# Performance work log

Measured on AMD Instinct MI355X. Metric: run time of the kernel, lower is better.

Reference implementation:

```python
import jax, jax.numpy as jnp
import numpy as np

EMBEDS = 195  # C, also used in the (unusual) 1/sqrt(C) scale


def setup_inputs() -> dict:
    key = jax.random.key(0)
    k1, k2, k3, k4 = jax.random.split(key, 4)
    B, T, C, H = 1024, 256, EMBEDS, 8
    x = jax.random.normal(k1, (B, T, C), dtype=jnp.float32)
    Wq = jax.random.normal(k2, (C, H), dtype=jnp.float32) * 0.05
    Wk = jax.random.normal(k3, (C, H), dtype=jnp.float32) * 0.05
    Wv = jax.random.normal(k4, (C, H), dtype=jnp.float32) * 0.05
    return {"x": x, "Wq": Wq, "Wk": Wk, "Wv": Wv}


def reference(x, Wq, Wk, Wv):
    B, T, C = x.shape
    q = jnp.einsum('btc,ch->bth', x, Wq)  # [B,T,H]
    k = jnp.einsum('btc,ch->bth', x, Wk)
    v = jnp.einsum('btc,ch->bth', x, Wv)
    # scores scaled by 1/sqrt(C) (embedding dim), faithful to source
    scores = jnp.einsum('bqh,bkh->bqk', q, k) * (1.0 / jnp.sqrt(jnp.float32(C)))
    causal = jnp.tril(jnp.ones((T, T), dtype=bool))  # [T,T]
    scores = jnp.where(causal, scores, -jnp.inf)
    attn = jax.nn.softmax(scores, axis=-1)
    # dropout treated as identity (eval mode) for deterministic reference
    out = jnp.einsum('bqk,bkh->bqh', attn, v)
    return out
```

## Files before the change

kernel.cpp:

```cpp
#include <hip/hip_runtime.h>
#include <hip/hip_bf16.h>
#include <stdint.h>

#define TT   256
#define CC   195
#define HH   8
#define NKT  7
#define VSTR 260
#define PSTR 40

typedef __attribute__((ext_vector_type(8))) short short8;
typedef __attribute__((ext_vector_type(4))) float f32x4;

static __device__ __forceinline__ short f2bf(float v) {
    union { __hip_bfloat16 h; short s; } cv;
    cv.h = __float2bfloat16(v);
    return cv.s;
}

__global__ __launch_bounds__(256, 4)
void fused_head(const float* __restrict__ x,
                const float* __restrict__ Wq,
                const float* __restrict__ Wk,
                const float* __restrict__ Wv,
                float* __restrict__ out)
{
    __shared__ short Ql[TT * 8];
    __shared__ short Kl[TT * 8];
    __shared__ short Vt[16 * VSTR];
    __shared__ short Pch[4 * 16 * PSTR];

    const int tid  = threadIdx.x;
    const int lane = tid & 63;
    const int wv   = __builtin_amdgcn_readfirstlane(tid >> 6);
    const int b    = blockIdx.x;
    const int nn   = lane & 15;
    const int quad = lane >> 4;

    {
        uint32_t* vtw = (uint32_t*)Vt;
        const int base = (8 * VSTR) / 2;
        for (int i = tid; i < (8 * VSTR) / 2; i += 256)
            vtw[base + i] = (i < VSTR / 2) ? 0x3F803F80u : 0u;
    }

    const float* __restrict__ xb = x + (size_t)b * (TT * CC);

    const float* Wsel0 = (nn < 8) ? (Wq + nn) : (Wk + nn - 8);
    const float* Wsel1 = (nn < 8) ? (Wv + nn) : nullptr;
    short8 Bf[NKT][2];
#pragma unroll
    for (int kt = 0; kt < NKT; ++kt) {
#pragma unroll
        for (int j = 0; j < 8; ++j) {
            const int k = kt * 32 + quad * 8 + j;
            float v0 = (k < CC) ? Wsel0[(size_t)k * HH] : 0.f;
            float v1 = (k < CC && Wsel1) ? Wsel1[(size_t)k * HH] : 0.f;
            Bf[kt][0][j] = f2bf(v0);
            Bf[kt][1][j] = f2bf(v1);
        }
    }

    for (int ch = 0; ch < 4; ++ch) {
        const int rbase = ch * 64 + wv * 16;
        const float* __restrict__ xrow = xb + (size_t)(rbase + nn) * CC;

        f32x4 acc0 = {0.f, 0.f, 0.f, 0.f};
        f32x4 acc1 = {0.f, 0.f, 0.f, 0.f};
#pragma unroll
        for (int kt = 0; kt < NKT; ++kt) {
            float f[8];
#pragma unroll
            for (int j = 0; j < 8; ++j) {
                const int k = kt * 32 + quad * 8 + j;
                f[j] = (k < CC) ? xrow[k] : 0.f;
            }
            short8 a;
#pragma unroll
            for (int j = 0; j < 8; ++j) a[j] = f2bf(f[j]);
            acc0 = __builtin_amdgcn_mfma_f32_16x16x32_bf16(a, Bf[kt][0], acc0, 0, 0, 0);
            acc1 = __builtin_amdgcn_mfma_f32_16x16x32_bf16(a, Bf[kt][1], acc1, 0, 0, 0);
        }
#pragma unroll
        for (int r = 0; r < 4; ++r) {
            const int trow = rbase + quad * 4 + r;
            const short qs = f2bf(acc0[r]);
            if (nn < 8) {
                Ql[trow * 8 + nn] = qs;
                Vt[nn * VSTR + trow] = f2bf(acc1[r]);
            } else {
                Kl[trow * 8 + (nn - 8)] = qs;
            }
        }
    }
    __syncthreads();

    const float SC2 = 0.07161149f * 1.44269504f;
    const int qt4[4] = { wv, 7 - wv, 8 + wv, 15 - wv };
    short* Pw = Pch + wv * (16 * PSTR);

    for (int qi = 0; qi < 4; ++qi) {
        const int qt = qt4[qi];
        const int qb = qt * 16;

        short8 aQ = (short8){0, 0, 0, 0, 0, 0, 0, 0};
        if (quad == 0)
            aQ = *reinterpret_cast<const short8*>(Ql + (qb + nn) * 8);

        f32x4 accO = {0.f, 0.f, 0.f, 0.f};
        const int nch = (qt >> 1) + 1;
        for (int c = 0; c < nch; ++c) {
            const int kb = c * 32;
            asm volatile("" ::: "memory");
#pragma unroll
            for (int half = 0; half < 2; ++half) {
                const int kb16 = kb + half * 16;
                short8 bK = (short8){0, 0, 0, 0, 0, 0, 0, 0};
                if (quad == 0)
                    bK = *reinterpret_cast<const short8*>(Kl + (kb16 + nn) * 8);
                f32x4 s = __builtin_amdgcn_mfma_f32_16x16x32_bf16(
                              aQ, bK, (f32x4){0.f, 0.f, 0.f, 0.f}, 0, 0, 0);
                const int key = kb16 + nn;
#pragma unroll
                for (int r = 0; r < 4; ++r) {
                    const int qrow = qb + quad * 4 + r;
                    const float e = (key <= qrow) ? exp2f(s[r] * SC2) : 0.f;
                    Pw[(quad * 4 + r) * PSTR + half * 16 + nn] = f2bf(e);
                }
            }
            asm volatile("s_waitcnt lgkmcnt(0)" ::: "memory");
            const short8 aP = *reinterpret_cast<const short8*>(Pw + nn * PSTR + quad * 8);
            const short8 bV = *reinterpret_cast<const short8*>(Vt + nn * VSTR + kb + quad * 8);
            accO = __builtin_amdgcn_mfma_f32_16x16x32_bf16(aP, bV, accO, 0, 0, 0);
        }
#pragma unroll
        for (int r = 0; r < 4; ++r) {
            const float dn = __shfl(accO[r], (lane & 48) | 8);
            if (nn < 8) {
                const int qrow = qb + quad * 4 + r;
                out[((size_t)b * TT + qrow) * HH + nn] = accO[r] / dn;
            }
        }
    }
}

extern "C" void kernel_launch(void* const* d_in, const int* in_sizes, int n_in,
                              void* d_out, int out_size, void* d_ws, size_t ws_size,
                              hipStream_t stream)
{
    const float* x  = (const float*)d_in[0];
    const float* Wq = (const float*)d_in[1];
    const float* Wk = (const float*)d_in[2];
    const float* Wv = (const float*)d_in[3];
    float* out      = (float*)d_out;
    const int B = in_sizes[0] / (TT * CC);
    fused_head<<<dim3(B), dim3(256), 0, stream>>>(x, Wq, Wk, Wv, out);
}
```

Baseline: 306.2 us.

## Split fused head into projection and attention kernels via workspace

Replaces the single per-batch fused kernel with two kernels. A projection kernel stages 64 rows of x in LDS as packed bf16 with coalesced loads, then writes Q/K and transposed V to a global workspace. An attention kernel, launched over two blocks per batch, reads them back and supplies the all-ones denominator column as a register constant. The goal is more parallelism and better-coalesced x loads, at the cost of an extra launch and a bf16 global round trip. The fused kernel remains as a fallback when the workspace is too small.

```diff
diff --git a/kernel.cpp b/kernel.cpp
--- a/kernel.cpp
+++ b/kernel.cpp
@@ -6,8 +6,9 @@
 #define CC   195
 #define HH   8
 #define NKT  7
+#define XSTR 200
+#define PSTR 40
 #define VSTR 260
-#define PSTR 40
 
 typedef __attribute__((ext_vector_type(8))) short short8;
 typedef __attribute__((ext_vector_type(4))) float f32x4;
@@ -16,6 +17,153 @@
     union { __hip_bfloat16 h; short s; } cv;
     cv.h = __float2bfloat16(v);
     return cv.s;
+}
+static __device__ __forceinline__ uint32_t pkbf2(float a, float b) {
+    return (uint32_t)(uint16_t)f2bf(a) | ((uint32_t)(uint16_t)f2bf(b) << 16);
+}
+
+__global__ __launch_bounds__(256, 5)
+void proj_kernel(const float* __restrict__ x,
+                 const float* __restrict__ Wq,
+                 const float* __restrict__ Wk,
+                 const float* __restrict__ Wv,
+                 short* __restrict__ qk_g,
+                 short* __restrict__ vt_g)
+{
+    __shared__ short xs[64 * XSTR];
+
+    const int tid  = threadIdx.x;
+    const int lane = tid & 63;
+    const int wv   = __builtin_amdgcn_readfirstlane(tid >> 6);
+    const int nn   = lane & 15;
+    const int quad = lane >> 4;
+    const size_t row0 = (size_t)blockIdx.x * 64;
+    const float* __restrict__ xb = x + row0 * CC;
+
+    const float* Wsel0 = (nn < 8) ? (Wq + nn) : (Wk + nn - 8);
+    const float* Wsel1 = (nn < 8) ? (Wv + nn) : nullptr;
+    short8 Bf[NKT][2];
+#pragma unroll
+    for (int kt = 0; kt < NKT; ++kt) {
+#pragma unroll
+        for (int j = 0; j < 8; ++j) {
+            const int k = kt * 32 + quad * 8 + j;
+            float v0 = (k < CC) ? Wsel0[(size_t)k * HH] : 0.f;
+            float v1 = (k < CC && Wsel1) ? Wsel1[(size_t)k * HH] : 0.f;
+            Bf[kt][0][j] = f2bf(v0);
+            Bf[kt][1][j] = f2bf(v1);
+        }
+    }
+
+    uint32_t* xsw = (uint32_t*)xs;
+    for (int it = 0; it < 25; ++it) {
+        const int w   = it * 256 + tid;
+        const int row = w / 100;
+        const int cp  = w - row * 100;
+        const int col = cp * 2;
+        const float f0 = (col     < CC) ? xb[row * CC + col]     : 0.f;
+        const float f1 = (col + 1 < CC) ? xb[row * CC + col + 1] : 0.f;
+        xsw[w] = pkbf2(f0, f1);
+    }
+    __syncthreads();
+
+    f32x4 acc0 = {0.f, 0.f, 0.f, 0.f};
+    f32x4 acc1 = {0.f, 0.f, 0.f, 0.f};
+    const short* arow = xs + (wv * 16 + nn) * XSTR;
+#pragma unroll
+    for (int kt = 0; kt < NKT; ++kt) {
+        short8 a = (short8){0, 0, 0, 0, 0, 0, 0, 0};
+        if (kt < 6 || quad == 0)
+            a = *reinterpret_cast<const short8*>(arow + kt * 32 + quad * 8);
+        acc0 = __builtin_amdgcn_mfma_f32_16x16x32_bf16(a, Bf[kt][0], acc0, 0, 0, 0);
+        acc1 = __builtin_amdgcn_mfma_f32_16x16x32_bf16(a, Bf[kt][1], acc1, 0, 0, 0);
+    }
+#pragma unroll
+    for (int r = 0; r < 4; ++r) {
+        const size_t trow = row0 + wv * 16 + quad * 4 + r;
+        qk_g[trow * 16 + nn] = f2bf(acc0[r]);
+        if (nn < 8) {
+            const size_t bb = trow >> 8;
+            const int    tt = (int)(trow & 255);
+            vt_g[(bb * 8 + nn) * 256 + tt] = f2bf(acc1[r]);
+        }
+    }
+}
+
+__global__ __launch_bounds__(256, 4)
+void attn_kernel(const short* __restrict__ qk_g,
+                 const short* __restrict__ vt_g,
+                 float* __restrict__ out)
+{
+    __shared__ short Pch[4 * 16 * PSTR];
+
+    const int tid  = threadIdx.x;
+    const int lane = tid & 63;
+    const int wv   = __builtin_amdgcn_readfirstlane(tid >> 6);
+    const int nn   = lane & 15;
+    const int quad = lane >> 4;
+    const int blk  = blockIdx.x;
+    const int b    = blk >> 1;
+    const int half = blk & 1;
+
+    const short* __restrict__ qkb = qk_g + (size_t)b * (TT * 16);
+    const short* __restrict__ vtb = vt_g + (size_t)b * (HH * TT);
+
+    short8 bVconst = (short8){0, 0, 0, 0, 0, 0, 0, 0};
+    if (nn == 8) {
+        const short one = (short)0x3F80;
+#pragma unroll
+        for (int j = 0; j < 8; ++j) bVconst[j] = one;
+    }
+
+    const float SC2 = 0.07161149f * 1.44269504f;
+    short* Pw = Pch + wv * (16 * PSTR);
+
+    for (int qi = 0; qi < 2; ++qi) {
+        const int qt = half * 8 + (qi ? 7 - wv : wv);
+        const int qb = qt * 16;
+
+        short8 aQ = (short8){0, 0, 0, 0, 0, 0, 0, 0};
+        if (quad == 0)
+            aQ = *reinterpret_cast<const short8*>(qkb + (qb + nn) * 16);
+
+        f32x4 accO = {0.f, 0.f, 0.f, 0.f};
+        const int nch = (qt >> 1) + 1;
+        for (int c = 0; c < nch; ++c) {
+            const int kb = c * 32;
+            asm volatile("" ::: "memory");
+#pragma unroll
+            for (int h2 = 0; h2 < 2; ++h2) {
+                const int kb16 = kb + h2 * 16;
+                short8 bK = (short8){0, 0, 0, 0, 0, 0, 0, 0};
+                if (quad == 0)
+                    bK = *reinterpret_cast<const short8*>(qkb + (kb16 + nn) * 16 + 8);
+                f32x4 s = __builtin_amdgcn_mfma_f32_16x16x32_bf16(
+                              aQ, bK, (f32x4){0.f, 0.f, 0.f, 0.f}, 0, 0, 0);
+                const int key = kb16 + nn;
+#pragma unroll
+                for (int r = 0; r < 4; ++r) {
+                    const int qrow = qb + quad * 4 + r;
+                    const float e = (key <= qrow) ? exp2f(s[r] * SC2) : 0.f;
+                    Pw[(quad * 4 + r) * PSTR + h2 * 16 + nn] = f2bf(e);
+                }
+            }
+            asm volatile("s_waitcnt lgkmcnt(0)" ::: "memory");
+            const short8 aP = *reinterpret_cast<const short8*>(Pw + nn * PSTR + quad * 8);
+            short8 bV = bVconst;
+            if (nn < 8)
+                bV = *reinterpret_cast<const short8*>(vtb + nn * TT + kb + quad * 8);
+            accO = __builtin_amdgcn_mfma_f32_16x16x32_bf16(aP, bV, accO, 0, 0, 0);
+        }
+#pragma unroll
+        for (int r = 0; r < 4; ++r) {
+            const float dn = __shfl(accO[r], (lane & 48) | 8);
+            if (nn < 8) {
+                const int qrow = qb + quad * 4 + r;
+                out[((size_t)b * TT + qrow) * HH + nn] = accO[r] / dn;
+            }
+        }
+    }
 }
 
 __global__ __launch_bounds__(256, 4)
@@ -45,7 +193,6 @@
     }
 
     const float* __restrict__ xb = x + (size_t)b * (TT * CC);
-
     const float* Wsel0 = (nn < 8) ? (Wq + nn) : (Wk + nn - 8);
     const float* Wsel1 = (nn < 8) ? (Wv + nn) : nullptr;
     short8 Bf[NKT][2];
@@ -64,7 +211,6 @@
     for (int ch = 0; ch < 4; ++ch) {
         const int rbase = ch * 64 + wv * 16;
         const float* __restrict__ xrow = xb + (size_t)(rbase + nn) * CC;
-
         f32x4 acc0 = {0.f, 0.f, 0.f, 0.f};
         f32x4 acc1 = {0.f, 0.f, 0.f, 0.f};
 #pragma unroll
@@ -102,19 +248,17 @@
     for (int qi = 0; qi < 4; ++qi) {
         const int qt = qt4[qi];
         const int qb = qt * 16;
-
         short8 aQ = (short8){0, 0, 0, 0, 0, 0, 0, 0};
         if (quad == 0)
             aQ = *reinterpret_cast<const short8*>(Ql + (qb + nn) * 8);
-
         f32x4 accO = {0.f, 0.f, 0.f, 0.f};
         const int nch = (qt >> 1) + 1;
         for (int c = 0; c < nch; ++c) {
             const int kb = c * 32;
             asm volatile("" ::: "memory");
 #pragma unroll
-            for (int half = 0; half < 2; ++half) {
-                const int kb16 = kb + half * 16;
+            for (int h2 = 0; h2 < 2; ++h2) {
+                const int kb16 = kb + h2 * 16;
                 short8 bK = (short8){0, 0, 0, 0, 0, 0, 0, 0};
                 if (quad == 0)
                     bK = *reinterpret_cast<const short8*>(Kl + (kb16 + nn) * 8);
@@ -125,7 +269,7 @@
                 for (int r = 0; r < 4; ++r) {
                     const int qrow = qb + quad * 4 + r;
                     const float e = (key <= qrow) ? exp2f(s[r] * SC2) : 0.f;
-                    Pw[(quad * 4 + r) * PSTR + half * 16 + nn] = f2bf(e);
+                    Pw[(quad * 4 + r) * PSTR + h2 * 16 + nn] = f2bf(e);
                 }
             }
             asm volatile("s_waitcnt lgkmcnt(0)" ::: "memory");
@@ -154,5 +298,14 @@
     const float* Wv = (const float*)d_in[3];
     float* out      = (float*)d_out;
     const int B = in_sizes[0] / (TT * CC);
-    fused_head<<<dim3(B), dim3(256), 0, stream>>>(x, Wq, Wk, Wv, out);
-}
+
+    const size_t need = (size_t)B * (TT * 16 + HH * TT) * sizeof(short);
+    if (ws_size >= need) {
+        short* qk_g = (short*)d_ws;
+        short* vt_g = qk_g + (size_t)B * TT * 16;
+        proj_kernel<<<dim3(B * 4), dim3(256), 0, stream>>>(x, Wq, Wk, Wv, qk_g, vt_g);
+        attn_kernel<<<dim3(B * 2), dim3(256), 0, stream>>>(qk_g, vt_g, out);
+    } else {
+        fused_head<<<dim3(B), dim3(256), 0, stream>>>(x, Wq, Wk, Wv, out);
+    }
+}
```

Result: slower. 443.5 us (+44.8%).

## Stage x slabs and weights through LDS with coalesced float4 loads

Applied to the files above, without the earlier changes.

Each wave now loads its 16-row x slab with contiguous float4 global reads, converts it to bf16 and writes it into padded LDS rows. The MFMA A fragments are then read from LDS instead of each lane doing eight strided scalar global loads. Weights are also loaded cooperatively into an LDS transpose rather than per-lane strided reads, and the P scratch reuses the x staging area. Total LDS grows to about 52KB, so launch bounds drop occupancy to 3 blocks per CU, and the extra LDS traffic and barriers may offset the coalescing gain.

```diff
diff --git a/kernel.cpp b/kernel.cpp
--- a/kernel.cpp
+++ b/kernel.cpp
@@ -6,7 +6,9 @@
 #define CC   195
 #define HH   8
 #define NKT  7
-#define VSTR 260
+#define XSTR 200
+#define WSTR 224
+#define VSTR 264
 #define PSTR 40
 
 typedef __attribute__((ext_vector_type(8))) short short8;
@@ -18,17 +20,25 @@
     return cv.s;
 }
 
-__global__ __launch_bounds__(256, 4)
+#define OFF_WT 25600
+#define OFF_QL 36352
+#define OFF_KL 40448
+#define OFF_VT 44544
+
+__global__ __launch_bounds__(256, 3)
 void fused_head(const float* __restrict__ x,
                 const float* __restrict__ Wq,
                 const float* __restrict__ Wk,
                 const float* __restrict__ Wv,
                 float* __restrict__ out)
 {
-    __shared__ short Ql[TT * 8];
-    __shared__ short Kl[TT * 8];
-    __shared__ short Vt[16 * VSTR];
-    __shared__ short Pch[4 * 16 * PSTR];
+    __shared__ __align__(16) char smem[52992];
+    short* xs = (short*)smem;
+    short* Wt = (short*)(smem + OFF_WT);
+    short* Ql = (short*)(smem + OFF_QL);
+    short* Kl = (short*)(smem + OFF_KL);
+    short* Vt = (short*)(smem + OFF_VT);
+    short* Pch = xs;
 
     const int tid  = threadIdx.x;
     const int lane = tid & 63;
@@ -37,47 +47,75 @@
     const int nn   = lane & 15;
     const int quad = lane >> 4;
 
+    const float* __restrict__ xb = x + (size_t)b * (TT * CC);
+
+    for (int i = tid; i < 24 * 32; i += 256) {
+        const int row = i >> 5, c = 192 + (i & 31);
+        if (c >= CC) Wt[row * WSTR + c] = 0;
+    }
     {
         uint32_t* vtw = (uint32_t*)Vt;
-        const int base = (8 * VSTR) / 2;
-        for (int i = tid; i < (8 * VSTR) / 2; i += 256)
-            vtw[base + i] = (i < VSTR / 2) ? 0x3F803F80u : 0u;
+        for (int i = tid; i < 8 * 128; i += 256) {
+            const int row = 8 + (i >> 7), w = i & 127;
+            vtw[row * (VSTR / 2) + w] = (row == 8) ? 0x3F803F80u : 0u;
+        }
     }
+    if (tid < 64) {
+        short* xr = xs + (tid >> 4) * (16 * XSTR) + (tid & 15) * XSTR;
+#pragma unroll
+        for (int j = CC; j < XSTR; ++j) xr[j] = 0;
+    }
+    for (int i = tid; i < 3 * CC * HH; i += 256) {
+        const int m = i / (CC * HH);
+        const int f = i - m * (CC * HH);
+        const int c = f >> 3, h = f & 7;
+        const float* Wp = (m == 0) ? Wq : (m == 1) ? Wk : Wv;
+        Wt[(m * 8 + h) * WSTR + c] = f2bf(Wp[f]);
+    }
+    __syncthreads();
 
-    const float* __restrict__ xb = x + (size_t)b * (TT * CC);
-
-    const float* Wsel0 = (nn < 8) ? (Wq + nn) : (Wk + nn - 8);
-    const float* Wsel1 = (nn < 8) ? (Wv + nn) : nullptr;
     short8 Bf[NKT][2];
 #pragma unroll
     for (int kt = 0; kt < NKT; ++kt) {
-#pragma unroll
-        for (int j = 0; j < 8; ++j) {
-            const int k = kt * 32 + quad * 8 + j;
-            float v0 = (k < CC) ? Wsel0[(size_t)k * HH] : 0.f;
-            float v1 = (k < CC && Wsel1) ? Wsel1[(size_t)k * HH] : 0.f;
-            Bf[kt][0][j] = f2bf(v0);
-            Bf[kt][1][j] = f2bf(v1);
-        }
+        Bf[kt][0] = *reinterpret_cast<const short8*>(Wt + nn * WSTR + kt * 32 + quad * 8);
+        Bf[kt][1] = (nn < 8)
+            ? *reinterpret_cast<const short8*>(Wt + (16 + nn) * WSTR + kt * 32 + quad * 8)
+            : (short8){0, 0, 0, 0, 0, 0, 0, 0};
     }
 
+    short* xw = xs + wv * (16 * XSTR);
     for (int ch = 0; ch < 4; ++ch) {
         const int rbase = ch * 64 + wv * 16;
-        const float* __restrict__ xrow = xb + (size_t)(rbase + nn) * CC;
+        const float4* slab = reinterpret_cast<const float4*>(xb + (size_t)rbase * CC);
+
+        asm volatile("s_waitcnt lgkmcnt(0)" ::: "memory");
+#pragma unroll
+        for (int i = 0; i < 13; ++i) {
+            const int idx = i * 64 + lane;
+            if (idx < (16 * CC) / 4) {
+                const float4 f = slab[idx];
+                const int fi  = idx * 4;
+                const int row = fi / 195;
+                const int c0  = fi - row * 195;
+                short* dst = xw + row * XSTR + c0;
+                const float fv[4] = {f.x, f.y, f.z, f.w};
+#pragma unroll
+                for (int j = 0; j < 4; ++j) {
+                    const int adj = (c0 + j >= CC) ? (XSTR - CC) : 0;
+                    dst[j + adj] = f2bf(fv[j]);
+                }
+            }
+        }
+        asm volatile("s_waitcnt lgkmcnt(0)" ::: "memory");
 
         f32x4 acc0 = {0.f, 0.f, 0.f, 0.f};
         f32x4 acc1 = {0.f, 0.f, 0.f, 0.f};
+        const short* arow = xw + nn * XSTR;
 #pragma unroll
         for (int kt = 0; kt < NKT; ++kt) {
-            float f[8];
-#pragma unroll
-            for (int j = 0; j < 8; ++j) {
-                const int k = kt * 32 + quad * 8 + j;
-                f[j] = (k < CC) ? xrow[k] : 0.f;
-            }
-            short8 a;
-#pragma unroll
-            for (int j = 0; j < 8; ++j) a[j] = f2bf(f[j]);
+            short8 a = (short8){0, 0, 0, 0, 0, 0, 0, 0};
+            if (kt < 6 || quad == 0)
+                a = *reinterpret_cast<const short8*>(arow + kt * 32 + quad * 8);
             acc0 = __builtin_amdgcn_mfma_f32_16x16x32_bf16(a, Bf[kt][0], acc0, 0, 0, 0);
             acc1 = __builtin_amdgcn_mfma_f32_16x16x32_bf16(a, Bf[kt][1], acc1, 0, 0, 0);
         }
@@ -113,8 +151,8 @@
             const int kb = c * 32;
             asm volatile("" ::: "memory");
 #pragma unroll
-            for (int half = 0; half < 2; ++half) {
-                const int kb16 = kb + half * 16;
+            for (int h2 = 0; h2 < 2; ++h2) {
+                const int kb16 = kb + h2 * 16;
                 short8 bK = (short8){0, 0, 0, 0, 0, 0, 0, 0};
                 if (quad == 0)
                     bK = *reinterpret_cast<const short8*>(Kl + (kb16 + nn) * 8);
@@ -125,7 +163,7 @@
                 for (int r = 0; r < 4; ++r) {
                     const int qrow = qb + quad * 4 + r;
                     const float e = (key <= qrow) ? exp2f(s[r] * SC2) : 0.f;
-                    Pw[(quad * 4 + r) * PSTR + half * 16 + nn] = f2bf(e);
+                    Pw[(quad * 4 + r) * PSTR + h2 * 16 + nn] = f2bf(e);
                 }
             }
             asm volatile("s_waitcnt lgkmcnt(0)" ::: "memory");
```

After: 321.5 us. +5.0%, slower.
